# Kernel optimization log

Measured on AMD Instinct MI355X. Metric: run time of the kernel, lower is better.

## Reference

```python
import jax, jax.numpy as jnp
import numpy as np

B, L, DIM, H = 2, 2048, 1024, 16
HD = DIM // H  # head dim = 64
MASK_SCALE = -10 * 6  # faithful to the original source: mask_expand *= -10 * 6


def setup_inputs() -> dict:
    key = jax.random.key(0)
    ks = jax.random.split(key, 8)
    s = 1.0 / np.sqrt(DIM)
    return {
        "x": jax.random.normal(ks[0], (B, L, DIM), jnp.float32),
        "attention_mask": jax.random.uniform(ks[1], (B, L, L), jnp.float32),
        "Wq": jax.random.normal(ks[2], (DIM, DIM), jnp.float32) * s,
        "bq": jnp.zeros((DIM,), jnp.float32),
        "Wk": jax.random.normal(ks[3], (DIM, DIM), jnp.float32) * s,
        "bk": jnp.zeros((DIM,), jnp.float32),
        "Wv": jax.random.normal(ks[4], (DIM, DIM), jnp.float32) * s,
        "bv": jnp.zeros((DIM,), jnp.float32),
    }


def _split_heads(t):
    # [B, L, DIM] -> [B, H, L, HD]
    return t.reshape(B, L, H, HD).transpose(0, 2, 1, 3)


def reference(x, attention_mask, Wq, bq, Wk, bk, Wv, bv):
    q = _split_heads(x @ Wq + bq)
    k = _split_heads(x @ Wk + bk)
    v = _split_heads(x @ Wv + bv)
    scale = float(HD) ** -0.5
    # full [B, H, L, L] score matrix, as in the original
    scores = jnp.einsum("bhqd,bhkd->bhqk", q, k) * scale
    scores = scores + attention_mask[:, None, :, :] * MASK_SCALE
    probs = jax.nn.softmax(scores, axis=-1)
    ctx = jnp.einsum("bhqk,bhkd->bhqd", probs, v)
    # merge heads back: [B, L, DIM]
    return ctx.transpose(0, 2, 1, 3).reshape(B, L, DIM)
```

## Files before the change

### kernel.cpp

```cpp
#include <hip/hip_runtime.h>

#define LL 2048
#define NHEADS 16
#define HDIM 64
#define QSCALE 0.18033688011112042f
#define MASKC1 -86.56170245333780f

typedef __attribute__((ext_vector_type(8))) __bf16 bf16x8;
typedef __attribute__((ext_vector_type(4))) float f32x4;
typedef __attribute__((ext_vector_type(4))) unsigned int u32x4;

__device__ __forceinline__ unsigned short f2bf(float f) {
  unsigned int u = __builtin_bit_cast(unsigned int, f);
  u += 0x7fffu + ((u >> 16) & 1u);
  return (unsigned short)(u >> 16);
}

__device__ __forceinline__ bf16x8 ld_frag(const unsigned short* p) {
  return *reinterpret_cast<const bf16x8*>(p);
}

__device__ __forceinline__ float bflo(unsigned int u) {
  return __builtin_bit_cast(float, u << 16);
}
__device__ __forceinline__ float bfhi(unsigned int u) {
  return __builtin_bit_cast(float, u & 0xffff0000u);
}
__device__ __forceinline__ unsigned int pack2(float hi, float lo) {
  return __builtin_amdgcn_perm(__builtin_bit_cast(unsigned int, hi),
                               __builtin_bit_cast(unsigned int, lo), 0x07060302u);
}

__device__ __forceinline__ void async_cp16(const unsigned short* g, unsigned short* l) {
  __builtin_amdgcn_global_load_lds(
      (const __attribute__((address_space(1))) unsigned int*)(unsigned long long)(g),
      (__attribute__((address_space(3))) unsigned int*)(unsigned int)(unsigned long long)(l),
      16, 0, 0);
}

__device__ __forceinline__ void lem_load(const unsigned short* p, uint4& a, uint4& b,
                                         uint4& c, uint4& d) {
  asm volatile("global_load_dwordx4 %0, %4, off\n\t"
               "global_load_dwordx4 %1, %4, off offset:16\n\t"
               "global_load_dwordx4 %2, %4, off offset:32\n\t"
               "global_load_dwordx4 %3, %4, off offset:48"
               : "=&v"(a), "=&v"(b), "=&v"(c), "=&v"(d)
               : "v"(p)
               : "memory");
}

__global__ __launch_bounds__(256) void prep_kernel(const float* __restrict__ x,
                                                   const float* __restrict__ Wq,
                                                   const float* __restrict__ Wk,
                                                   const float* __restrict__ Wv,
                                                   unsigned short* __restrict__ xb,
                                                   unsigned short* __restrict__ WtAll) {
  const int z = blockIdx.z;
  if (z == 3) {
    const int bidx = blockIdx.y * 16 + blockIdx.x;
    const int base = bidx * 256 + threadIdx.x;
#pragma unroll
    for (int p = 0; p < 16; ++p) {
      int i = (p * 65536 + base) * 4;
      float4 v = *reinterpret_cast<const float4*>(x + i);
      ushort4 o;
      o.x = f2bf(v.x); o.y = f2bf(v.y); o.z = f2bf(v.z); o.w = f2bf(v.w);
      *reinterpret_cast<ushort4*>(xb + i) = o;
    }
    return;
  }
  const float* W = (z == 0) ? Wq : (z == 1) ? Wk : Wv;
  unsigned short* dst = WtAll + (size_t)z * 1024 * 1024;
  int n0 = blockIdx.x * 64, k0 = blockIdx.y * 64;
  __shared__ float t[64][65];
  int tx = threadIdx.x & 63, ty = threadIdx.x >> 6;
#pragma unroll
  for (int p = 0; p < 16; ++p) {
    int kr = p * 4 + ty;
    t[kr][tx] = W[(size_t)(k0 + kr) * 1024 + n0 + tx];
  }
  __syncthreads();
#pragma unroll
  for (int p = 0; p < 16; ++p) {
    int nr = p * 4 + ty;
    dst[(size_t)(n0 + nr) * 1024 + k0 + tx] = f2bf(t[tx][nr]);
  }
}

__global__ __launch_bounds__(256) void lem_prep_kernel(const float* __restrict__ mask,
                                                       unsigned short* __restrict__ lem) {
  const int qb = blockIdx.x, kt = blockIdx.y, b = blockIdx.z;
  const int tid = threadIdx.x;
  __shared__ unsigned short lds[128 * 72];
  {
    const int r0 = tid >> 4;
    const int c0 = (tid & 15) * 4;
#pragma unroll
    for (int p = 0; p < 8; ++p) {
      int row = p * 16 + r0;
      float4 v = *reinterpret_cast<const float4*>(
          mask + ((size_t)b * LL + qb * 128 + row) * LL + kt * 64 + c0);
      ushort4 o;
      o.x = f2bf(v.x * MASKC1); o.y = f2bf(v.y * MASKC1);
      o.z = f2bf(v.z * MASKC1); o.w = f2bf(v.w * MASKC1);
      *reinterpret_cast<ushort4*>(&lds[row * 72 + c0]) = o;
    }
  }
  __syncthreads();
  const int w = tid >> 6, lane = tid & 63, g = lane >> 4, cc = lane & 15;
  unsigned int ow[16];
#pragma unroll
  for (int mt = 0; mt < 2; ++mt) {
    const int q = w * 32 + mt * 16 + cc;
#pragma unroll
    for (int nt = 0; nt < 4; ++nt) {
      uint2 v = *reinterpret_cast<const uint2*>(&lds[q * 72 + nt * 16 + g * 4]);
      ow[mt * 8 + nt * 2]     = v.x;
      ow[mt * 8 + nt * 2 + 1] = v.y;
    }
  }
  uint4* dst = reinterpret_cast<uint4*>(
      lem + ((((size_t)b * 16 + qb) * 32 + kt) * 256 + tid) * 32);
#pragma unroll
  for (int j = 0; j < 4; ++j)
    dst[j] = make_uint4(ow[4 * j], ow[4 * j + 1], ow[4 * j + 2], ow[4 * j + 3]);
}

__global__ __launch_bounds__(256) void qkv_gemm_kernel(
    const unsigned short* __restrict__ xb, const unsigned short* __restrict__ WtAll,
    const float* __restrict__ bq, const float* __restrict__ bk, const float* __restrict__ bv,
    unsigned short* __restrict__ qkv) {
  const int z = blockIdx.z;
  const unsigned short* Wt = WtAll + (size_t)z * 1024 * 1024;
  const float* bias = (z == 0) ? bq : (z == 1) ? bk : bv;
  unsigned short* outb = qkv + (size_t)z * 4194304;

  __shared__ __align__(16) unsigned short smem[16384];
  unsigned short* As = smem;
  unsigned short* Bs = smem + 8192;

  const int tid = threadIdx.x;
  const int w = tid >> 6, lane = tid & 63, g = lane >> 4, cc = lane & 15;
  const int wm = w >> 1, wn = w & 1;
  const int m0 = blockIdx.y * 128, n0 = blockIdx.x * 128;
  const int srow = lane >> 3;
  const int gc = ((lane & 7) - srow) & 7;
  const unsigned short* ga = xb + (size_t)(m0 + w * 32 + srow) * 1024 + gc * 8;
  const unsigned short* gb = Wt + (size_t)(n0 + w * 32 + srow) * 1024 + gc * 8;
  unsigned short* la = As + w * 2048;
  unsigned short* lb = Bs + w * 2048;

  f32x4 acc[4][4];
#pragma unroll
  for (int i = 0; i < 4; ++i)
#pragma unroll
    for (int j = 0; j < 4; ++j) acc[i][j] = (f32x4)0.0f;

  for (int kk = 0; kk < 1024; kk += 64) {
    __syncthreads();
#pragma unroll
    for (int i = 0; i < 4; ++i) {
      async_cp16(ga + i * 8192 + kk, la + i * 512);
      async_cp16(gb + i * 8192 + kk, lb + i * 512);
    }
    __syncthreads();
    bf16x8 af[4][2], bfr[4][2];
#pragma unroll
    for (int mt = 0; mt < 4; ++mt)
#pragma unroll
      for (int ks = 0; ks < 2; ++ks)
        af[mt][ks] = ld_frag(&As[(wm * 64 + mt * 16 + cc) * 64 + ((4 * ks + g + cc) & 7) * 8]);
#pragma unroll
    for (int nt = 0; nt < 4; ++nt)
#pragma unroll
      for (int ks = 0; ks < 2; ++ks)
        bfr[nt][ks] = ld_frag(&Bs[(wn * 64 + nt * 16 + cc) * 64 + ((4 * ks + g + cc) & 7) * 8]);
#pragma unroll
    for (int mt = 0; mt < 4; ++mt)
#pragma unroll
      for (int nt = 0; nt < 4; ++nt)
#pragma unroll
        for (int ks = 0; ks < 2; ++ks)
          acc[mt][nt] = __builtin_amdgcn_mfma_f32_16x16x32_bf16(af[mt][ks], bfr[nt][ks],
                                                                acc[mt][nt], 0, 0, 0);
  }

  if (z != 2) {
    const float sc = (z == 0) ? QSCALE : 1.0f;
#pragma unroll
    for (int nt = 0; nt < 4; ++nt) {
      int n = n0 + wn * 64 + nt * 16 + cc;
      float bval = bias[n];
      int h = n >> 6, d = n & 63;
#pragma unroll
      for (int mt = 0; mt < 4; ++mt) {
#pragma unroll
        for (int r = 0; r < 4; ++r) {
          int m = m0 + wm * 64 + mt * 16 + g * 4 + r;
          int b = m >> 11, l = m & 2047;
          outb[(((size_t)(b * NHEADS + h) * LL) + l) * HDIM + d] =
              f2bf((acc[mt][nt][r] + bval) * sc);
        }
      }
    }
  } else {
    __syncthreads();
#pragma unroll
    for (int nt = 0; nt < 4; ++nt) {
      int nr = wn * 64 + nt * 16 + cc;
      float bval = bias[n0 + nr];
#pragma unroll
      for (int mt = 0; mt < 4; ++mt)
#pragma unroll
        for (int r = 0; r < 4; ++r)
          smem[nr * 128 + wm * 64 + (mt >> 1) * 32 + g * 8 + (mt & 1) * 4 + r] =
              f2bf(acc[mt][nt][r] + bval);
    }
    __syncthreads();
    int row = tid >> 1, half = tid & 1;
    int n = n0 + row, hh = n >> 6, dd = n & 63;
    int bb = m0 >> 11, l0 = (m0 & 2047) + half * 64;
    unsigned short* dst = outb + ((size_t)(bb * NHEADS + hh) * HDIM + dd) * LL + l0;
#pragma unroll
    for (int i = 0; i < 8; ++i)
      *reinterpret_cast<uint4*>(dst + i * 8) =
          *reinterpret_cast<const uint4*>(&smem[row * 128 + half * 64 + i * 8]);
  }
}

__global__ __launch_bounds__(256, 2) void flash_kernel(
    const unsigned short* __restrict__ Qb, const unsigned short* __restrict__ Kb,
    const unsigned short* __restrict__ Vt, const unsigned short* __restrict__ Lem,
    float* __restrict__ out) {
  const int id = blockIdx.y * 16 + blockIdx.x;
  const int nid = (id & 7) * 64 + (id >> 3);
  const int qb = nid & 15, bh = nid >> 4;
  const int b = bh >> 4, h = bh & 15;
  const int q0 = qb * 128;
  const int tid = threadIdx.x, w = tid >> 6, lane = tid & 63, g = lane >> 4, cc = lane & 15;
  const size_t bhoff = (size_t)bh * LL * HDIM;

  __shared__ __align__(16) unsigned short Ks[3][64 * 64];
  __shared__ __align__(16) unsigned short Vs[3][64 * 64];

  bf16x8 aq[2][2];
#pragma unroll
  for (int mt = 0; mt < 2; ++mt)
#pragma unroll
    for (int ks = 0; ks < 2; ++ks)
      aq[mt][ks] = *reinterpret_cast<const bf16x8*>(
          Qb + bhoff + (size_t)(q0 + w * 32 + mt * 16 + cc) * HDIM + ks * 32 + g * 8);

  const int srow = lane >> 3;
  const int gcs = ((lane & 7) - srow) & 7;
  const unsigned short* kg0 = Kb + bhoff + (size_t)(w * 8 + srow) * HDIM + gcs * 8;
  const unsigned short* kg1 = Kb + bhoff + (size_t)(32 + w * 8 + srow) * HDIM + gcs * 8;
  const unsigned short* vg0 = Vt + bhoff + (size_t)(w * 8 + srow) * LL + gcs * 8;
  const unsigned short* vg1 = Vt + bhoff + (size_t)(32 + w * 8 + srow) * LL + gcs * 8;

  const unsigned short* lemq = Lem + (((size_t)b * 16 + qb) * 32 * 256 + tid) * 32;

  const u32x4 onesu = {0x3F803F80u, 0x3F803F80u, 0x3F803F80u, 0x3F803F80u};
  const bf16x8 bones = __builtin_bit_cast(bf16x8, onesu);

  uint4 l00, l01, l02, l03, l10, l11, l12, l13, l20, l21, l22, l23;

  f32x4 liacc[2];
  f32x4 oacc[2][4];
#pragma unroll
  for (int mt = 0; mt < 2; ++mt) {
    liacc[mt] = (f32x4)0.0f;
#pragma unroll
    for (int nt = 0; nt < 4; ++nt) oacc[mt][nt] = (f32x4)0.0f;
  }

  async_cp16(kg0, Ks[0] + w * 512);
  async_cp16(kg1, Ks[0] + (w + 4) * 512);
  async_cp16(vg0, Vs[0] + w * 512);
  async_cp16(vg1, Vs[0] + (w + 4) * 512);
  lem_load(lemq, l00, l01, l02, l03);
  lemq += 8192;
  async_cp16(kg0 + (size_t)64 * HDIM, Ks[1] + w * 512);
  async_cp16(kg1 + (size_t)64 * HDIM, Ks[1] + (w + 4) * 512);
  async_cp16(vg0 + 64, Vs[1] + w * 512);
  async_cp16(vg1 + 64, Vs[1] + (w + 4) * 512);
  lem_load(lemq, l10, l11, l12, l13);
  lemq += 8192;

#define FLASH_COMPUTE(BUF, LSA, LSB, LSC, LSD)                                         \
  {                                                                                    \
    bf16x8 bk_[4][2], bv[4][2];                                                        \
    _Pragma("unroll") for (int nt = 0; nt < 4; ++nt)                                   \
      _Pragma("unroll") for (int ks = 0; ks < 2; ++ks)                                 \
        bk_[nt][ks] =                                                                  \
            ld_frag(&Ks[BUF][(nt * 16 + cc) * 64 + ((4 * ks + g + cc) & 7) * 8]);      \
    _Pragma("unroll") for (int nt = 0; nt < 4; ++nt)                                   \
      _Pragma("unroll") for (int ks = 0; ks < 2; ++ks)                                 \
        bv[nt][ks] =                                                                   \
            ld_frag(&Vs[BUF][(nt * 16 + cc) * 64 + ((4 * ks + g + cc) & 7) * 8]);      \
    bf16x8 ap[2][2];                                                                   \
    _Pragma("unroll") for (int mt = 0; mt < 2; ++mt) {                                 \
      f32x4 sacc[4];                                                                   \
      const uint4 ea = (mt == 0) ? LSA : LSC;                                          \
      const uint4 eb = (mt == 0) ? LSB : LSD;                                          \
      sacc[0][0] = bflo(ea.x); sacc[0][1] = bfhi(ea.x);                                \
      sacc[0][2] = bflo(ea.y); sacc[0][3] = bfhi(ea.y);                                \
      sacc[1][0] = bflo(ea.z); sacc[1][1] = bfhi(ea.z);                                \
      sacc[1][2] = bflo(ea.w); sacc[1][3] = bfhi(ea.w);                                \
      sacc[2][0] = bflo(eb.x); sacc[2][1] = bfhi(eb.x);                                \
      sacc[2][2] = bflo(eb.y); sacc[2][3] = bfhi(eb.y);                                \
      sacc[3][0] = bflo(eb.z); sacc[3][1] = bfhi(eb.z);                                \
      sacc[3][2] = bflo(eb.w); sacc[3][3] = bfhi(eb.w);                                \
      _Pragma("unroll") for (int nt = 0; nt < 4; ++nt)                                 \
        _Pragma("unroll") for (int ks = 0; ks < 2; ++ks)                               \
          sacc[nt] = __builtin_amdgcn_mfma_f32_16x16x32_bf16(bk_[nt][ks], aq[mt][ks],  \
                                                             sacc[nt], 0, 0, 0);       \
      float p[4][4];                                                                   \
      _Pragma("unroll") for (int nt = 0; nt < 4; ++nt)                                 \
        _Pragma("unroll") for (int r = 0; r < 4; ++r)                                  \
          p[nt][r] = __builtin_amdgcn_exp2f(sacc[nt][r]);                              \
      unsigned int wd[8];                                                              \
      _Pragma("unroll") for (int ks = 0; ks < 2; ++ks) {                               \
        wd[ks * 4 + 0] = pack2(p[2 * ks][1],     p[2 * ks][0]);                        \
        wd[ks * 4 + 1] = pack2(p[2 * ks][3],     p[2 * ks][2]);                        \
        wd[ks * 4 + 2] = pack2(p[2 * ks + 1][1], p[2 * ks + 1][0]);                    \
        wd[ks * 4 + 3] = pack2(p[2 * ks + 1][3], p[2 * ks + 1][2]);                    \
        u32x4 uv = {wd[ks * 4], wd[ks * 4 + 1], wd[ks * 4 + 2], wd[ks * 4 + 3]};       \
        ap[mt][ks] = __builtin_bit_cast(bf16x8, uv);                                   \
      }                                                                                \
    }                                                                                  \
    _Pragma("unroll") for (int mt = 0; mt < 2; ++mt) {                                 \
      _Pragma("unroll") for (int nt = 0; nt < 4; ++nt)                                 \
        _Pragma("unroll") for (int ks = 0; ks < 2; ++ks)                               \
          oacc[mt][nt] = __builtin_amdgcn_mfma_f32_16x16x32_bf16(ap[mt][ks], bv[nt][ks],\
                                                                 oacc[mt][nt], 0, 0, 0);\
      _Pragma("unroll") for (int ks = 0; ks < 2; ++ks)                                 \
        liacc[mt] = __builtin_amdgcn_mfma_f32_16x16x32_bf16(ap[mt][ks], bones,         \
                                                            liacc[mt], 0, 0, 0);       \
    }                                                                                  \
  }

#define FITER(KT, CBUF, SBUF, VMC, ISSUE, UA, UB, UC, UD, LA, LB, LC, LD)              \
  {                                                                                    \
    asm volatile("s_waitcnt vmcnt(" VMC ")" ::: "memory");                             \
    __builtin_amdgcn_sched_barrier(0);                                                 \
    asm volatile("s_barrier" ::: "memory");                                            \
    __builtin_amdgcn_sched_barrier(0);                                                 \
    if (ISSUE) {                                                                       \
      const size_t ko = (size_t)((KT) + 2) * 64;                                       \
      async_cp16(kg0 + ko * HDIM, Ks[SBUF] + w * 512);                                 \
      async_cp16(kg1 + ko * HDIM, Ks[SBUF] + (w + 4) * 512);                           \
      async_cp16(vg0 + ko, Vs[SBUF] + w * 512);                                        \
      async_cp16(vg1 + ko, Vs[SBUF] + (w + 4) * 512);                                  \
      lem_load(lemq, LA, LB, LC, LD);                                                  \
      lemq += 8192;                                                                    \
    }                                                                                  \
    FLASH_COMPUTE(CBUF, UA, UB, UC, UD);                                               \
  }

  for (int kt = 0; kt < 30; kt += 3) {
    FITER(kt + 0, 0, 2, "8", true,  l00, l01, l02, l03, l20, l21, l22, l23)
    FITER(kt + 1, 1, 0, "8", true,  l10, l11, l12, l13, l00, l01, l02, l03)
    FITER(kt + 2, 2, 1, "8", true,  l20, l21, l22, l23, l10, l11, l12, l13)
  }
  FITER(30, 0, 0, "8", false, l00, l01, l02, l03, l00, l01, l02, l03)
  FITER(31, 1, 0, "0", false, l10, l11, l12, l13, l10, l11, l12, l13)

#undef FITER
#undef FLASH_COMPUTE

#pragma unroll
  for (int mt = 0; mt < 2; ++mt) {
#pragma unroll
    for (int r = 0; r < 4; ++r) {
      float inv = 1.0f / liacc[mt][r];
      int qrow = q0 + w * 32 + mt * 16 + g * 4 + r;
#pragma unroll
      for (int nt = 0; nt < 4; ++nt)
        out[((size_t)b * LL + qrow) * 1024 + h * 64 + nt * 16 + cc] = oacc[mt][nt][r] * inv;
    }
  }
}

extern "C" void kernel_launch(void* const* d_in, const int* in_sizes, int n_in,
                              void* d_out, int out_size, void* d_ws, size_t ws_size,
                              hipStream_t stream) {
  const float* x    = (const float*)d_in[0];
  const float* mask = (const float*)d_in[1];
  const float* Wq   = (const float*)d_in[2];
  const float* bq   = (const float*)d_in[3];
  const float* Wk   = (const float*)d_in[4];
  const float* bk   = (const float*)d_in[5];
  const float* Wv   = (const float*)d_in[6];
  const float* bv   = (const float*)d_in[7];
  float* out = (float*)d_out;
  (void)in_sizes; (void)n_in; (void)out_size; (void)ws_size;

  char* ws = (char*)d_ws;
  unsigned short* qkv = (unsigned short*)(ws);
  unsigned short* xb  = (unsigned short*)(ws + (24u << 20));
  unsigned short* Wt  = (unsigned short*)(ws + (32u << 20));
  unsigned short* lem = (unsigned short*)(ws + (24u << 20));

  prep_kernel<<<dim3(16, 16, 4), dim3(256), 0, stream>>>(x, Wq, Wk, Wv, xb, Wt);
  qkv_gemm_kernel<<<dim3(8, 32, 3), dim3(256), 0, stream>>>(xb, Wt, bq, bk, bv, qkv);
  lem_prep_kernel<<<dim3(16, 32, 2), dim3(256), 0, stream>>>(mask, lem);
  flash_kernel<<<dim3(16, 32), dim3(256), 0, stream>>>(qkv, qkv + 4194304, qkv + 8388608,
                                                       lem, out);
}
```

Measured before the change: 203.3 us.

## Double-buffer QKV GEMM LDS tiles with async prefetch two stages ahead

The QKV projection GEMM now uses two LDS buffers and issues async global-to-LDS copies for the k-tile two steps ahead while computing on the current one. Explicit vmcnt waits and raw s_barrier replace the paired __syncthreads. The aim is to hide global load latency behind the MFMA work. In exchange LDS use doubles to 64KB per block, which may lower occupancy, and the hand-written wait counts must match the number of outstanding copies exactly.

After: 188.4 us. 1.08x faster.

```diff
diff --git a/kernel.cpp b/kernel.cpp
--- a/kernel.cpp
+++ b/kernel.cpp
@@ -135,9 +135,7 @@
   const float* bias = (z == 0) ? bq : (z == 1) ? bk : bv;
   unsigned short* outb = qkv + (size_t)z * 4194304;
 
-  __shared__ __align__(16) unsigned short smem[16384];
-  unsigned short* As = smem;
-  unsigned short* Bs = smem + 8192;
+  __shared__ __align__(16) unsigned short smem[32768];
 
   const int tid = threadIdx.x;
   const int w = tid >> 6, lane = tid & 63, g = lane >> 4, cc = lane & 15;
@@ -147,8 +145,6 @@
   const int gc = ((lane & 7) - srow) & 7;
   const unsigned short* ga = xb + (size_t)(m0 + w * 32 + srow) * 1024 + gc * 8;
   const unsigned short* gb = Wt + (size_t)(n0 + w * 32 + srow) * 1024 + gc * 8;
-  unsigned short* la = As + w * 2048;
-  unsigned short* lb = Bs + w * 2048;
 
   f32x4 acc[4][4];
 #pragma unroll
@@ -156,34 +152,57 @@
 #pragma unroll
     for (int j = 0; j < 4; ++j) acc[i][j] = (f32x4)0.0f;
 
-  for (int kk = 0; kk < 1024; kk += 64) {
-    __syncthreads();
-#pragma unroll
-    for (int i = 0; i < 4; ++i) {
-      async_cp16(ga + i * 8192 + kk, la + i * 512);
-      async_cp16(gb + i * 8192 + kk, lb + i * 512);
-    }
-    __syncthreads();
-    bf16x8 af[4][2], bfr[4][2];
-#pragma unroll
-    for (int mt = 0; mt < 4; ++mt)
-#pragma unroll
-      for (int ks = 0; ks < 2; ++ks)
-        af[mt][ks] = ld_frag(&As[(wm * 64 + mt * 16 + cc) * 64 + ((4 * ks + g + cc) & 7) * 8]);
-#pragma unroll
-    for (int nt = 0; nt < 4; ++nt)
-#pragma unroll
-      for (int ks = 0; ks < 2; ++ks)
-        bfr[nt][ks] = ld_frag(&Bs[(wn * 64 + nt * 16 + cc) * 64 + ((4 * ks + g + cc) & 7) * 8]);
-#pragma unroll
-    for (int mt = 0; mt < 4; ++mt)
-#pragma unroll
-      for (int nt = 0; nt < 4; ++nt)
-#pragma unroll
-        for (int ks = 0; ks < 2; ++ks)
-          acc[mt][nt] = __builtin_amdgcn_mfma_f32_16x16x32_bf16(af[mt][ks], bfr[nt][ks],
-                                                                acc[mt][nt], 0, 0, 0);
-  }
+#pragma unroll
+  for (int i = 0; i < 4; ++i) {
+    async_cp16(ga + i * 8192, smem + w * 2048 + i * 512);
+    async_cp16(gb + i * 8192, smem + 8192 + w * 2048 + i * 512);
+  }
+#pragma unroll
+  for (int i = 0; i < 4; ++i) {
+    async_cp16(ga + i * 8192 + 64, smem + 16384 + w * 2048 + i * 512);
+    async_cp16(gb + i * 8192 + 64, smem + 24576 + w * 2048 + i * 512);
+  }
+
+#define QITER(KT, BUF, VMC, ISSUE)                                                     \
+  {                                                                                    \
+    asm volatile("s_waitcnt vmcnt(" VMC ")" ::: "memory");                             \
+    asm volatile("s_barrier" ::: "memory");                                            \
+    {                                                                                  \
+      const unsigned short* Ab = smem + (BUF) * 16384;                                 \
+      const unsigned short* Bb = smem + (BUF) * 16384 + 8192;                          \
+      bf16x8 af[4][2], bfr[4][2];                                                      \
+      _Pragma("unroll") for (int mt = 0; mt < 4; ++mt)                                 \
+        _Pragma("unroll") for (int ks = 0; ks < 2; ++ks)                               \
+          af[mt][ks] =                                                                 \
+              ld_frag(&Ab[(wm * 64 + mt * 16 + cc) * 64 + ((4 * ks + g + cc) & 7) * 8]);\
+      _Pragma("unroll") for (int nt = 0; nt < 4; ++nt)                                 \
+        _Pragma("unroll") for (int ks = 0; ks < 2; ++ks)                               \
+          bfr[nt][ks] =                                                                \
+              ld_frag(&Bb[(wn * 64 + nt * 16 + cc) * 64 + ((4 * ks + g + cc) & 7) * 8]);\
+      _Pragma("unroll") for (int mt = 0; mt < 4; ++mt)                                 \
+        _Pragma("unroll") for (int nt = 0; nt < 4; ++nt)                               \
+          _Pragma("unroll") for (int ks = 0; ks < 2; ++ks)                             \
+            acc[mt][nt] = __builtin_amdgcn_mfma_f32_16x16x32_bf16(af[mt][ks], bfr[nt][ks],\
+                                                                  acc[mt][nt], 0, 0, 0);\
+    }                                                                                  \
+    asm volatile("s_barrier" ::: "memory");                                            \
+    if (ISSUE) {                                                                       \
+      _Pragma("unroll") for (int i = 0; i < 4; ++i) {                                  \
+        async_cp16(ga + i * 8192 + ((KT) + 2) * 64, smem + (BUF) * 16384 + w * 2048 + i * 512);\
+        async_cp16(gb + i * 8192 + ((KT) + 2) * 64,                                    \
+                   smem + (BUF) * 16384 + 8192 + w * 2048 + i * 512);                  \
+      }                                                                                \
+    }                                                                                  \
+  }
+
+  for (int kt = 0; kt < 14; kt += 2) {
+    QITER(kt + 0, 0, "8", true)
+    QITER(kt + 1, 1, "8", true)
+  }
+  QITER(14, 0, "8", false)
+  QITER(15, 1, "0", false)
+
+#undef QITER
 
   if (z != 2) {
     const float sc = (z == 0) ? QSCALE : 1.0f;
```
